# Performance work log

Hardware: AMD Instinct MI355X
Metric: run time of the kernel (lower is better)

## Reference

```python
import jax, jax.numpy as jnp
import numpy as np

NUM_HEADS = 12

def setup_inputs() -> dict:
    key = jax.random.key(0)
    k1, k2, k3 = jax.random.split(key, 3)
    B, T, C = 1, 4096, 768
    x = jax.random.normal(k1, (B, T, C), dtype=jnp.float32)
    w_qkv = jax.random.normal(k2, (3 * C, C), dtype=jnp.float32) * (1.0 / np.sqrt(C))
    w_proj = jax.random.normal(k3, (C, C), dtype=jnp.float32) * (1.0 / np.sqrt(C))
    attn_mask = jnp.tril(jnp.ones((T, T), dtype=bool))  # causal block mask
    return {"x": x, "w_qkv": w_qkv, "w_proj": w_proj, "attn_mask": attn_mask}


def reference(x, w_qkv, w_proj, attn_mask):
    B, T, C = x.shape
    H = NUM_HEADS
    Dh = C // H
    # fused QKV projection (torch Linear: y = x @ W.T), then split
    qkv = jnp.einsum('btc,fc->btf', x, w_qkv)  # [B,T,3C]
    q, k, v = jnp.split(qkv, 3, axis=-1)
    # [B,T,C] -> [B,H,T,Dh]
    q = q.reshape(B, T, H, Dh).transpose(0, 2, 1, 3)
    k = k.reshape(B, T, H, Dh).transpose(0, 2, 1, 3)
    v = v.reshape(B, T, H, Dh).transpose(0, 2, 1, 3)
    # masked SDPA, default flex_attention scale = 1/sqrt(head_dim)
    scores = jnp.einsum('bhqd,bhkd->bhqk', q, k) * (1.0 / np.sqrt(Dh))
    neg = jnp.finfo(scores.dtype).min
    scores = jnp.where(attn_mask[None, None, :, :], scores, neg)
    attn = jax.nn.softmax(scores, axis=-1)
    y = jnp.einsum('bhqk,bhkd->bhqd', attn, v)
    # [B,H,T,Dh] -> [B,T,C], then output projection (dropout=0)
    y = y.transpose(0, 2, 1, 3).reshape(B, T, C)
    y = jnp.einsum('btc,fc->btf', y, w_proj)
    return y
```

## Files before the change

kernel.cpp:

```cpp
#include <hip/hip_runtime.h>

typedef unsigned short u16;
typedef unsigned int u32;
typedef __attribute__((ext_vector_type(8))) short s16x8;
typedef __attribute__((ext_vector_type(4))) float f32x4;
typedef __attribute__((ext_vector_type(4))) u16 u16x4;
typedef __attribute__((ext_vector_type(4))) u32 u32x4;

#define LOG2E 1.4426950408889634f

#if __has_builtin(__builtin_amdgcn_exp2f)
#define EXP2F __builtin_amdgcn_exp2f
#else
#define EXP2F exp2f
#endif

__device__ __forceinline__ u16 f32_to_bf16(float f) {
  union { float f; u32 u; } c; c.f = f;
  return (u16)((c.u + 0x7fffu + ((c.u >> 16) & 1u)) >> 16);
}

__device__ __forceinline__ u32 cvtpk(float lo, float hi) {
  u32 r;
  asm("v_cvt_pk_bf16_f32 %0, %1, %2" : "=v"(r) : "v"(lo), "v"(hi));
  return r;
}

__device__ __forceinline__ void async16(const void* g, void* l) {
  __builtin_amdgcn_global_load_lds(
      (__attribute__((address_space(1))) void*)g,
      (__attribute__((address_space(3))) void*)l, 16, 0, 0);
}

__global__ __launch_bounds__(256) void cast3_f32_bf16(const float* __restrict__ a,
                                                      const float* __restrict__ b,
                                                      const float* __restrict__ c,
                                                      u16* __restrict__ out,
                                                      int n1, int n2, int n3) {
  int i = (blockIdx.x * 256 + threadIdx.x) * 4;
  const float* src;
  int off = i;
  if (i < n1) {
    src = a;
  } else if (i < n1 + n2) {
    src = b; off = i - n1;
  } else if (i < n1 + n2 + n3) {
    src = c; off = i - n1 - n2;
  } else {
    return;
  }
  f32x4 v = *(const f32x4*)(src + off);
  u16x4 o;
  o[0] = f32_to_bf16(v[0]);
  o[1] = f32_to_bf16(v[1]);
  o[2] = f32_to_bf16(v[2]);
  o[3] = f32_to_bf16(v[3]);
  *(u16x4*)(out + i) = o;
}

__device__ __forceinline__ int vt_perm_inv(int k) {
  return (k & 35) | ((k & 16) >> 2) | ((k & 12) << 1);
}

__global__ __launch_bounds__(512) void qkv_gemm(const u16* __restrict__ A,
                                                const u16* __restrict__ B,
                                                u16* __restrict__ qk,
                                                u16* __restrict__ vt) {
  constexpr int K = 768;
  constexpr int BK = 32;
  constexpr int NT = K / BK;
  __shared__ alignas(16) u16 As[2][128 * BK];
  __shared__ alignas(16) u16 Bs[2][128 * BK];
  const int tid = threadIdx.x;
  const int lane = tid & 63;
  const int wid = tid >> 6;
  const int brow = blockIdx.x * 128;
  const int bcol = blockIdx.y * 128;
  const int wr = wid >> 2, wc = wid & 3;
  const int l15 = lane & 15, l4 = lane >> 4;
  f32x4 acc[4][2] = {};
  const int r0 = tid >> 2, s0 = tid & 3;

#define G1_STAGE(kt, b)                                                         \
  {                                                                             \
    async16(A + (size_t)(brow + r0) * K + (kt) * BK + s0 * 8, &As[b][tid * 8]); \
    async16(B + (size_t)(bcol + r0) * K + (kt) * BK + s0 * 8, &Bs[b][tid * 8]); \
  }

  G1_STAGE(0, 0);
  __syncthreads();
  int cur = 0;
  for (int kt = 0; kt < NT; ++kt) {
    if (kt + 1 < NT) G1_STAGE(kt + 1, cur ^ 1);
    s16x8 af[4], bf[2];
#pragma unroll
    for (int m = 0; m < 4; ++m)
      af[m] = *(const s16x8*)&As[cur][(wr * 64 + m * 16 + l15) * BK + l4 * 8];
#pragma unroll
    for (int n = 0; n < 2; ++n)
      bf[n] = *(const s16x8*)&Bs[cur][(wc * 32 + n * 16 + l15) * BK + l4 * 8];
#pragma unroll
    for (int m = 0; m < 4; ++m)
#pragma unroll
      for (int n = 0; n < 2; ++n)
        acc[m][n] = __builtin_amdgcn_mfma_f32_16x16x32_bf16(af[m], bf[n], acc[m][n], 0, 0, 0);
    __syncthreads();
    cur ^= 1;
  }
#undef G1_STAGE

  const int row0 = brow + wr * 64 + l4 * 4;
  const int col0 = bcol + wc * 32 + l15;
  if (bcol >= 1536) {
#pragma unroll
    for (int m = 0; m < 4; ++m) {
      int t0 = row0 + m * 16;
      int s = (t0 & ~63) + vt_perm_inv(t0 & 63);
#pragma unroll
      for (int n = 0; n < 2; ++n) {
        int vcol = col0 + n * 16 - 1536;
        u16x4 pk;
#pragma unroll
        for (int r = 0; r < 4; ++r) pk[r] = f32_to_bf16(acc[m][n][r]);
        *(u16x4*)&vt[(size_t)vcol * 4096 + s] = pk;
      }
    }
  } else {
    const float qs = (bcol < 768) ? 0.125f * LOG2E : 1.0f;
#pragma unroll
    for (int m = 0; m < 4; ++m)
#pragma unroll
      for (int n = 0; n < 2; ++n)
#pragma unroll
        for (int r = 0; r < 4; ++r)
          qk[(size_t)(row0 + m * 16 + r) * 1536 + (col0 + n * 16)] =
              f32_to_bf16(acc[m][n][r] * qs);
  }
}

__global__ __launch_bounds__(256) void proj_gemm(const u16* __restrict__ A,
                                                 const u16* __restrict__ B,
                                                 float* __restrict__ C) {
  constexpr int K = 768;
  constexpr int N = 768;
  constexpr int BK = 32;
  constexpr int NT = K / BK;
  __shared__ alignas(16) u16 As[2][64 * BK];
  __shared__ alignas(16) u16 Bs[2][64 * BK];
  const int tid = threadIdx.x;
  const int lane = tid & 63;
  const int wid = tid >> 6;
  const int brow = blockIdx.x * 64;
  const int bcol = blockIdx.y * 64;
  const int wr = wid >> 1, wc = wid & 1;
  const int l15 = lane & 15, l4 = lane >> 4;
  f32x4 acc[2][2] = {};
  const int r0 = tid >> 2, s0 = tid & 3;

#define G2_STAGE(kt, b)                                                         \
  {                                                                             \
    async16(A + (size_t)(brow + r0) * K + (kt) * BK + s0 * 8, &As[b][tid * 8]); \
    async16(B + (size_t)(bcol + r0) * K + (kt) * BK + s0 * 8, &Bs[b][tid * 8]); \
  }

  G2_STAGE(0, 0);
  __syncthreads();
  int cur = 0;
  for (int kt = 0; kt < NT; ++kt) {
    if (kt + 1 < NT) G2_STAGE(kt + 1, cur ^ 1);
    s16x8 af[2], bf[2];
#pragma unroll
    for (int m = 0; m < 2; ++m)
      af[m] = *(const s16x8*)&As[cur][(wr * 32 + m * 16 + l15) * BK + l4 * 8];
#pragma unroll
    for (int n = 0; n < 2; ++n)
      bf[n] = *(const s16x8*)&Bs[cur][(wc * 32 + n * 16 + l15) * BK + l4 * 8];
#pragma unroll
    for (int m = 0; m < 2; ++m)
#pragma unroll
      for (int n = 0; n < 2; ++n)
        acc[m][n] = __builtin_amdgcn_mfma_f32_16x16x32_bf16(af[m], bf[n], acc[m][n], 0, 0, 0);
    __syncthreads();
    cur ^= 1;
  }
#undef G2_STAGE

  const int row0 = brow + wr * 32 + l4 * 4;
  const int col0 = bcol + wc * 32 + l15;
#pragma unroll
  for (int m = 0; m < 2; ++m)
#pragma unroll
    for (int n = 0; n < 2; ++n)
#pragma unroll
      for (int r = 0; r < 4; ++r)
        C[(size_t)(row0 + m * 16 + r) * N + (col0 + n * 16)] = acc[m][n][r];
}

constexpr int cph_for(int C) {
  int s = 0;
  for (int qb = 0; qb < 32; ++qb) s += (2 * qb + 2 + C - 1) / C;
  return s;
}

template <int C>
__global__ __launch_bounds__(256) void attn_kernel(const u16* __restrict__ qk,
                                                   const u16* __restrict__ vt,
                                                   u16* __restrict__ y,
                                                   float* __restrict__ po,
                                                   float* __restrict__ pl) {
  constexpr int MAXCH = (64 + C - 1) / C;
  constexpr int CPH = cph_for(C);
  __shared__ alignas(16) u16 Ks[2][64 * 64];
  __shared__ alignas(16) u16 Vs[2][64 * 64];
  const int tid = threadIdx.x;
  const int lane = tid & 63;
  const int wid = tid >> 6;
  const int l15 = lane & 15, l4 = lane >> 4;

  const int h = blockIdx.x % 12;
  int c = CPH - 1 - (int)(blockIdx.x / 12);
  int qb = 0, ch = c;
  for (;;) {
    int n = (2 * qb + 2 + C - 1) / C;
    if (ch < n) break;
    ch -= n;
    ++qb;
  }
  const int NTt = 2 * qb + 2;
  const int nch = (NTt + C - 1) / C;

  const int qw0 = qb * 128 + wid * 32;

  s16x8 bq[2][2];
#pragma unroll
  for (int qf = 0; qf < 2; ++qf)
#pragma unroll
    for (int ks = 0; ks < 2; ++ks)
      bq[qf][ks] = *(const s16x8*)&qk[(size_t)(qw0 + qf * 16 + l15) * 1536 +
                                      h * 64 + ks * 32 + l4 * 8];

  f32x4 o[2][4] = {};
  f32x4 lacc[2] = {};

  const u16* Kb = qk + 768 + h * 64;
  const u16* Vb = vt + (size_t)(h * 64) * 4096;

  const int sc0 = tid, sc1 = tid + 256;
  const int sr0 = sc0 >> 3, sp0 = sc0 & 7;
  const int sr1 = sc1 >> 3, sp1 = sc1 & 7;

#define STAGE_KV(t, b)                                                                        \
  {                                                                                           \
    async16(Kb + (size_t)((t) * 64 + sr0) * 1536 + ((sp0 ^ (sr0 & 7)) * 8), &Ks[b][sc0 * 8]); \
    async16(Kb + (size_t)((t) * 64 + sr1) * 1536 + ((sp1 ^ (sr1 & 7)) * 8), &Ks[b][sc1 * 8]); \
    async16(Vb + (size_t)sr0 * 4096 + (t) * 64 + ((sp0 ^ (sr0 & 7)) * 8), &Vs[b][sc0 * 8]);   \
    async16(Vb + (size_t)sr1 * 4096 + (t) * 64 + ((sp1 ^ (sr1 & 7)) * 8), &Vs[b][sc1 * 8]);   \
  }

  const int t0 = ch * C;
  const int t1 = (t0 + C < NTt) ? t0 + C : NTt;
  STAGE_KV(t0, 0);
  __syncthreads();
  int cur = 0;
  for (int kt = t0; kt < t1; ++kt) {
    if (kt + 1 < t1) STAGE_KV(kt + 1, cur ^ 1);

    f32x4 s4[2][4];
    __builtin_amdgcn_s_setprio(1);
#pragma unroll
    for (int kf = 0; kf < 4; ++kf) {
      int r = kf * 16 + l15;
      s16x8 k0 = *(const s16x8*)&Ks[cur][r * 64 + ((l4 ^ (r & 7)) * 8)];
      s16x8 k1 = *(const s16x8*)&Ks[cur][r * 64 + (((l4 + 4) ^ (r & 7)) * 8)];
#pragma unroll
      for (int qf = 0; qf < 2; ++qf) {
        f32x4 a = {};
        a = __builtin_amdgcn_mfma_f32_16x16x32_bf16(k0, bq[qf][0], a, 0, 0, 0);
        a = __builtin_amdgcn_mfma_f32_16x16x32_bf16(k1, bq[qf][1], a, 0, 0, 0);
        s4[qf][kf] = a;
      }
    }
    __builtin_amdgcn_s_setprio(0);
    if (kt >= 2 * qb) {
#pragma unroll
      for (int qf = 0; qf < 2; ++qf) {
        int qg = qw0 + qf * 16 + l15;
#pragma unroll
        for (int kf = 0; kf < 4; ++kf)
#pragma unroll
          for (int r = 0; r < 4; ++r)
            if (kt * 64 + kf * 16 + l4 * 4 + r > qg) s4[qf][kf][r] = -1e30f;
      }
    }
    u32 w[2][4][2];
#pragma unroll
    for (int qf = 0; qf < 2; ++qf)
#pragma unroll
      for (int kf = 0; kf < 4; ++kf) {
        f32x4 p;
#pragma unroll
        for (int r = 0; r < 4; ++r) p[r] = EXP2F(s4[qf][kf][r]);
        lacc[qf] += p;
        w[qf][kf][0] = cvtpk(p[0], p[1]);
        w[qf][kf][1] = cvtpk(p[2], p[3]);
      }
    __builtin_amdgcn_s_setprio(1);
#pragma unroll
    for (int ks2 = 0; ks2 < 2; ++ks2) {
      s16x8 bp[2];
#pragma unroll
      for (int qf = 0; qf < 2; ++qf) {
        u32x4 bu;
        bu[0] = w[qf][2 * ks2][0];
        bu[1] = w[qf][2 * ks2][1];
        bu[2] = w[qf][2 * ks2 + 1][0];
        bu[3] = w[qf][2 * ks2 + 1][1];
        bp[qf] = __builtin_bit_cast(s16x8, bu);
      }
#pragma unroll
      for (int df = 0; df < 4; ++df) {
        int d = df * 16 + l15;
        int e = ks2 * 4 + l4;
        s16x8 av = *(const s16x8*)&Vs[cur][d * 64 + ((e ^ (d & 7)) * 8)];
#pragma unroll
        for (int qf = 0; qf < 2; ++qf)
          o[qf][df] = __builtin_amdgcn_mfma_f32_16x16x32_bf16(av, bp[qf], o[qf][df], 0, 0, 0);
      }
    }
    __builtin_amdgcn_s_setprio(0);
    __syncthreads();
    cur ^= 1;
  }
#undef STAGE_KV

  float lsum[2];
#pragma unroll
  for (int qf = 0; qf < 2; ++qf) {
    float s = lacc[qf][0] + lacc[qf][1] + lacc[qf][2] + lacc[qf][3];
    s += __shfl_xor(s, 16);
    s += __shfl_xor(s, 32);
    lsum[qf] = s;
  }

  if (nch == 1) {
#pragma unroll
    for (int qf = 0; qf < 2; ++qf) {
      float inv = 1.0f / lsum[qf];
#pragma unroll
      for (int df = 0; df < 4; ++df) {
        u16x4 pk;
#pragma unroll
        for (int r = 0; r < 4; ++r) pk[r] = f32_to_bf16(o[qf][df][r] * inv);
        *(u16x4*)&y[(size_t)(qw0 + qf * 16 + l15) * 768 + h * 64 + df * 16 + l4 * 4] = pk;
      }
    }
  } else {
    const size_t slot = (size_t)(h * 32 + qb) * MAXCH + ch;
#pragma unroll
    for (int qf = 0; qf < 2; ++qf) {
      float* ob = po + slot * 8192 + (size_t)(wid * 32 + qf * 16 + l15) * 64;
#pragma unroll
      for (int df = 0; df < 4; ++df)
        *(f32x4*)(ob + df * 16 + l4 * 4) = o[qf][df];
      if (lane < 16) pl[slot * 128 + wid * 32 + qf * 16 + l15] = lsum[qf];
    }
  }
}

template <int C>
__global__ __launch_bounds__(256) void attn_combine(const float* __restrict__ po,
                                                    const float* __restrict__ pl,
                                                    u16* __restrict__ y) {
  constexpr int MAXCH = (64 + C - 1) / C;
  const int h = blockIdx.x;
  const int qb = blockIdx.y;
  const int nch = (2 * qb + 2 + C - 1) / C;
  if (nch == 1) return;
  const int tid = threadIdx.x;
  const int q = tid >> 1;
  const int d0 = (tid & 1) * 32;

  f32x4 acc[8] = {};
  float lt = 0.f;
  for (int s = 0; s < nch; ++s) {
    const size_t slot = (size_t)(h * 32 + qb) * MAXCH + s;
    lt += pl[slot * 128 + q];
    const float* ob = po + slot * 8192 + (size_t)q * 64 + d0;
#pragma unroll
    for (int j = 0; j < 8; ++j) acc[j] += *(const f32x4*)(ob + j * 4);
  }
  float inv = 1.0f / lt;
  u16* yp = &y[(size_t)(qb * 128 + q) * 768 + h * 64 + d0];
#pragma unroll
  for (int j = 0; j < 8; ++j) {
    u16x4 pk;
#pragma unroll
    for (int r = 0; r < 4; ++r) pk[r] = f32_to_bf16(acc[j][r] * inv);
    *(u16x4*)(yp + j * 4) = pk;
  }
}

extern "C" void kernel_launch(void* const* d_in, const int* in_sizes, int n_in,
                              void* d_out, int out_size, void* d_ws, size_t ws_size,
                              hipStream_t stream) {
  const float* x = (const float*)d_in[0];
  const float* w_qkv = (const float*)d_in[1];
  const float* w_proj = (const float*)d_in[2];
  float* out = (float*)d_out;

  u16* ws = (u16*)d_ws;
  u16* xb = ws;
  u16* wqkvb = xb + 4096 * 768;
  u16* wprojb = wqkvb + 2304 * 768;
  u16* qkb = wprojb + 768 * 768;
  u16* vtb = qkb + (size_t)4096 * 1536;
  u16* yb = vtb + (size_t)768 * 4096;
  const size_t base_u16 = (size_t)4096 * 768 + 2304 * 768 + 768 * 768 +
                          (size_t)4096 * 1536 + (size_t)768 * 4096 + (size_t)4096 * 768;
  float* pf = (float*)(ws + base_u16);
  const size_t base_b = base_u16 * 2;

  constexpr int N1 = 4096 * 768, N2 = 2304 * 768, N3 = 768 * 768;
  cast3_f32_bf16<<<(N1 + N2 + N3) / 4 / 256, 256, 0, stream>>>(
      x, w_qkv, w_proj, xb, N1, N2, N3);

  qkv_gemm<<<dim3(32, 18), 512, 0, stream>>>(xb, wqkvb, qkb, vtb);

  const size_t need8 = base_b + (size_t)(12 * 32 * 8) * (8192 + 128) * 4;
  const size_t need16 = base_b + (size_t)(12 * 32 * 4) * (8192 + 128) * 4;
  const size_t need32 = base_b + (size_t)(12 * 32 * 2) * (8192 + 128) * 4;
  if (ws_size >= need8) {
    constexpr int C = 8, MAXCH = 8;
    float* po = pf;
    float* pl = po + (size_t)12 * 32 * MAXCH * 8192;
    attn_kernel<C><<<12 * cph_for(C), 256, 0, stream>>>(qkb, vtb, yb, po, pl);
    attn_combine<C><<<dim3(12, 32), 256, 0, stream>>>(po, pl, yb);
  } else if (ws_size >= need16) {
    constexpr int C = 16, MAXCH = 4;
    float* po = pf;
    float* pl = po + (size_t)12 * 32 * MAXCH * 8192;
    attn_kernel<C><<<12 * cph_for(C), 256, 0, stream>>>(qkb, vtb, yb, po, pl);
    attn_combine<C><<<dim3(12, 32), 256, 0, stream>>>(po, pl, yb);
  } else if (ws_size >= need32) {
    constexpr int C = 32, MAXCH = 2;
    float* po = pf;
    float* pl = po + (size_t)12 * 32 * MAXCH * 8192;
    attn_kernel<C><<<12 * cph_for(C), 256, 0, stream>>>(qkb, vtb, yb, po, pl);
    attn_combine<C><<<dim3(12, 32), 256, 0, stream>>>(po, pl, yb);
  } else {
    constexpr int C = 64;
    attn_kernel<C><<<12 * cph_for(C), 256, 0, stream>>>(qkb, vtb, yb, nullptr, nullptr);
  }

  proj_gemm<<<dim3(64, 12), 256, 0, stream>>>(yb, wprojb, out);
}
```

Baseline: 113.3 us.

## Swizzle GEMM block order, store attention partials in bf16, compute row sums via MFMA

Both GEMMs remap block indices so consecutive workgroups cover different tiles, aiming to improve L2 reuse across CUs. The split-K attention partial outputs are stored as bf16 instead of fp32, halving the partial write/read traffic in the attention and combine kernels. Softmax row sums are now computed by an extra MFMA against a ones vector instead of vector adds and cross-lane shuffles. The bf16 partials lose some precision before the final normalization, and the extra MFMA adds matrix-unit work.

```diff
diff --git a/kernel.cpp b/kernel.cpp
--- a/kernel.cpp
+++ b/kernel.cpp
@@ -5,6 +5,7 @@
 typedef __attribute__((ext_vector_type(8))) short s16x8;
 typedef __attribute__((ext_vector_type(4))) float f32x4;
 typedef __attribute__((ext_vector_type(4))) u16 u16x4;
+typedef __attribute__((ext_vector_type(8))) u16 u16x8;
 typedef __attribute__((ext_vector_type(4))) u32 u32x4;
 
 #define LOG2E 1.4426950408889634f
@@ -18,6 +19,11 @@
 __device__ __forceinline__ u16 f32_to_bf16(float f) {
   union { float f; u32 u; } c; c.f = f;
   return (u16)((c.u + 0x7fffu + ((c.u >> 16) & 1u)) >> 16);
+}
+
+__device__ __forceinline__ float bf16_to_f32(u16 v) {
+  union { u32 u; float f; } c; c.u = (u32)v << 16;
+  return c.f;
 }
 
 __device__ __forceinline__ u32 cvtpk(float lo, float hi) {
@@ -74,8 +80,10 @@
   const int tid = threadIdx.x;
   const int lane = tid & 63;
   const int wid = tid >> 6;
-  const int brow = blockIdx.x * 128;
-  const int bcol = blockIdx.y * 128;
+  const int lid = blockIdx.y * 32 + blockIdx.x;
+  const int swz = (lid & 7) * 72 + (lid >> 3);
+  const int brow = (swz & 31) * 128;
+  const int bcol = (swz >> 5) * 128;
   const int wr = wid >> 2, wc = wid & 3;
   const int l15 = lane & 15, l4 = lane >> 4;
   f32x4 acc[4][2] = {};
@@ -150,8 +158,10 @@
   const int tid = threadIdx.x;
   const int lane = tid & 63;
   const int wid = tid >> 6;
-  const int brow = blockIdx.x * 64;
-  const int bcol = blockIdx.y * 64;
+  const int lid = blockIdx.y * 64 + blockIdx.x;
+  const int swz = (lid & 7) * 96 + (lid >> 3);
+  const int brow = (swz & 63) * 64;
+  const int bcol = (swz >> 6) * 64;
   const int wr = wid >> 1, wc = wid & 1;
   const int l15 = lane & 15, l4 = lane >> 4;
   f32x4 acc[2][2] = {};
@@ -206,7 +216,7 @@
 __global__ __launch_bounds__(256) void attn_kernel(const u16* __restrict__ qk,
                                                    const u16* __restrict__ vt,
                                                    u16* __restrict__ y,
-                                                   float* __restrict__ po,
+                                                   u16* __restrict__ po,
                                                    float* __restrict__ pl) {
   constexpr int MAXCH = (64 + C - 1) / C;
   constexpr int CPH = cph_for(C);
@@ -239,8 +249,11 @@
       bq[qf][ks] = *(const s16x8*)&qk[(size_t)(qw0 + qf * 16 + l15) * 1536 +
                                       h * 64 + ks * 32 + l4 * 8];
 
+  const short oval = (l15 == 0) ? (short)0x3F80 : (short)0;
+  const s16x8 aone = {oval, oval, oval, oval, oval, oval, oval, oval};
+
   f32x4 o[2][4] = {};
-  f32x4 lacc[2] = {};
+  f32x4 lv[2] = {};
 
   const u16* Kb = qk + 768 + h * 64;
   const u16* Vb = vt + (size_t)(h * 64) * 4096;
@@ -300,7 +313,6 @@
         f32x4 p;
 #pragma unroll
         for (int r = 0; r < 4; ++r) p[r] = EXP2F(s4[qf][kf][r]);
-        lacc[qf] += p;
         w[qf][kf][0] = cvtpk(p[0], p[1]);
         w[qf][kf][1] = cvtpk(p[2], p[3]);
       }
@@ -326,6 +338,9 @@
         for (int qf = 0; qf < 2; ++qf)
           o[qf][df] = __builtin_amdgcn_mfma_f32_16x16x32_bf16(av, bp[qf], o[qf][df], 0, 0, 0);
       }
+#pragma unroll
+      for (int qf = 0; qf < 2; ++qf)
+        lv[qf] = __builtin_amdgcn_mfma_f32_16x16x32_bf16(aone, bp[qf], lv[qf], 0, 0, 0);
     }
     __builtin_amdgcn_s_setprio(0);
     __syncthreads();
@@ -335,12 +350,8 @@
 
   float lsum[2];
 #pragma unroll
-  for (int qf = 0; qf < 2; ++qf) {
-    float s = lacc[qf][0] + lacc[qf][1] + lacc[qf][2] + lacc[qf][3];
-    s += __shfl_xor(s, 16);
-    s += __shfl_xor(s, 32);
-    lsum[qf] = s;
-  }
+  for (int qf = 0; qf < 2; ++qf)
+    lsum[qf] = __shfl(lv[qf][0], l15);
 
   if (nch == 1) {
 #pragma unroll
@@ -358,17 +369,21 @@
     const size_t slot = (size_t)(h * 32 + qb) * MAXCH + ch;
 #pragma unroll
     for (int qf = 0; qf < 2; ++qf) {
-      float* ob = po + slot * 8192 + (size_t)(wid * 32 + qf * 16 + l15) * 64;
-#pragma unroll
-      for (int df = 0; df < 4; ++df)
-        *(f32x4*)(ob + df * 16 + l4 * 4) = o[qf][df];
+      u16* ob = po + slot * 8192 + (size_t)(wid * 32 + qf * 16 + l15) * 64;
+#pragma unroll
+      for (int df = 0; df < 4; ++df) {
+        u16x4 pk;
+#pragma unroll
+        for (int r = 0; r < 4; ++r) pk[r] = f32_to_bf16(o[qf][df][r]);
+        *(u16x4*)(ob + df * 16 + l4 * 4) = pk;
+      }
       if (lane < 16) pl[slot * 128 + wid * 32 + qf * 16 + l15] = lsum[qf];
     }
   }
 }
 
 template <int C>
-__global__ __launch_bounds__(256) void attn_combine(const float* __restrict__ po,
+__global__ __launch_bounds__(256) void attn_combine(const u16* __restrict__ po,
                                                     const float* __restrict__ pl,
                                                     u16* __restrict__ y) {
   constexpr int MAXCH = (64 + C - 1) / C;
@@ -380,14 +395,18 @@
   const int q = tid >> 1;
   const int d0 = (tid & 1) * 32;
 
-  f32x4 acc[8] = {};
+  float acc[32] = {};
   float lt = 0.f;
   for (int s = 0; s < nch; ++s) {
     const size_t slot = (size_t)(h * 32 + qb) * MAXCH + s;
     lt += pl[slot * 128 + q];
-    const float* ob = po + slot * 8192 + (size_t)q * 64 + d0;
-#pragma unroll
-    for (int j = 0; j < 8; ++j) acc[j] += *(const f32x4*)(ob + j * 4);
+    const u16* ob = po + slot * 8192 + (size_t)q * 64 + d0;
+#pragma unroll
+    for (int j = 0; j < 4; ++j) {
+      u16x8 v = *(const u16x8*)(ob + j * 8);
+#pragma unroll
+      for (int e = 0; e < 8; ++e) acc[j * 8 + e] += bf16_to_f32(v[e]);
+    }
   }
   float inv = 1.0f / lt;
   u16* yp = &y[(size_t)(qb * 128 + q) * 768 + h * 64 + d0];
@@ -395,7 +414,7 @@
   for (int j = 0; j < 8; ++j) {
     u16x4 pk;
 #pragma unroll
-    for (int r = 0; r < 4; ++r) pk[r] = f32_to_bf16(acc[j][r] * inv);
+    for (int r = 0; r < 4; ++r) pk[r] = f32_to_bf16(acc[j * 4 + r] * inv);
     *(u16x4*)(yp + j * 4) = pk;
   }
 }
@@ -417,7 +436,7 @@
   u16* yb = vtb + (size_t)768 * 4096;
   const size_t base_u16 = (size_t)4096 * 768 + 2304 * 768 + 768 * 768 +
                           (size_t)4096 * 1536 + (size_t)768 * 4096 + (size_t)4096 * 768;
-  float* pf = (float*)(ws + base_u16);
+  u16* pbase = ws + base_u16;
   const size_t base_b = base_u16 * 2;
 
   constexpr int N1 = 4096 * 768, N2 = 2304 * 768, N3 = 768 * 768;
@@ -426,25 +445,25 @@
 
   qkv_gemm<<<dim3(32, 18), 512, 0, stream>>>(xb, wqkvb, qkb, vtb);
 
-  const size_t need8 = base_b + (size_t)(12 * 32 * 8) * (8192 + 128) * 4;
-  const size_t need16 = base_b + (size_t)(12 * 32 * 4) * (8192 + 128) * 4;
-  const size_t need32 = base_b + (size_t)(12 * 32 * 2) * (8192 + 128) * 4;
+  const size_t need8 = base_b + (size_t)(12 * 32 * 8) * (16384 + 512);
+  const size_t need16 = base_b + (size_t)(12 * 32 * 4) * (16384 + 512);
+  const size_t need32 = base_b + (size_t)(12 * 32 * 2) * (16384 + 512);
   if (ws_size >= need8) {
     constexpr int C = 8, MAXCH = 8;
-    float* po = pf;
-    float* pl = po + (size_t)12 * 32 * MAXCH * 8192;
+    u16* po = pbase;
+    float* pl = (float*)(po + (size_t)12 * 32 * MAXCH * 8192);
     attn_kernel<C><<<12 * cph_for(C), 256, 0, stream>>>(qkb, vtb, yb, po, pl);
     attn_combine<C><<<dim3(12, 32), 256, 0, stream>>>(po, pl, yb);
   } else if (ws_size >= need16) {
     constexpr int C = 16, MAXCH = 4;
-    float* po = pf;
-    float* pl = po + (size_t)12 * 32 * MAXCH * 8192;
+    u16* po = pbase;
+    float* pl = (float*)(po + (size_t)12 * 32 * MAXCH * 8192);
     attn_kernel<C><<<12 * cph_for(C), 256, 0, stream>>>(qkb, vtb, yb, po, pl);
     attn_combine<C><<<dim3(12, 32), 256, 0, stream>>>(po, pl, yb);
   } else if (ws_size >= need32) {
     constexpr int C = 32, MAXCH = 2;
-    float* po = pf;
-    float* pl = po + (size_t)12 * 32 * MAXCH * 8192;
+    u16* po = pbase;
+    float* pl = (float*)(po + (size_t)12 * 32 * MAXCH * 8192);
     attn_kernel<C><<<12 * cph_for(C), 256, 0, stream>>>(qkb, vtb, yb, po, pl);
     attn_combine<C><<<dim3(12, 32), 256, 0, stream>>>(po, pl, yb);
   } else {
```

New measurement: 108.2 us, median of 3. 1.05x faster.
